# Performance work log

Measured on AMD Instinct MI355X. Metric: run time of the kernel, lower is better.

Reference implementation:

```python
import jax, jax.numpy as jnp
import numpy as np

N, E, R, B, DIN, H1, H2 = 50000, 1000000, 8, 30, 64, 64, 64


def setup_inputs() -> dict:
    key = jax.random.key(0)
    ks = jax.random.split(key, 12)
    node_features = jax.random.normal(ks[0], (N, DIN), dtype=jnp.float32)
    src = jax.random.randint(ks[1], (E,), 0, N)
    dst = jax.random.randint(ks[2], (E,), 0, N)
    edge_index = jnp.stack([src, dst]).astype(jnp.int64)
    edge_norm = jax.random.uniform(ks[3], (E,), dtype=jnp.float32)
    edge_type = jax.random.randint(ks[4], (E,), 0, R).astype(jnp.int64)
    s = 0.05  # param init scale
    basis = jax.random.normal(ks[5], (B, DIN, H1), dtype=jnp.float32) * s
    comp = jax.random.normal(ks[6], (R, B), dtype=jnp.float32) * s
    loop_weight = jax.random.normal(ks[7], (DIN, H1), dtype=jnp.float32) * s
    bias1 = jnp.zeros((H1,), dtype=jnp.float32)
    weight2 = jax.random.normal(ks[8], (H1, H2), dtype=jnp.float32) * s
    bias2 = jnp.zeros((H2,), dtype=jnp.float32)
    return dict(node_features=node_features, edge_index=edge_index,
                edge_norm=edge_norm, edge_type=edge_type, basis=basis,
                comp=comp, loop_weight=loop_weight, bias1=bias1,
                weight2=weight2, bias2=bias2)


def reference(node_features, edge_index, edge_norm, edge_type, basis, comp,
              loop_weight, bias1, weight2, bias2):
    n = node_features.shape[0]
    src, dst = edge_index[0], edge_index[1]

    # ---- RGCNConv (basis decomposition, sum aggregation, self-loop, bias) ----
    # relation weights from bases: [R, DIN, H1]
    Wrel = jnp.einsum('rb,bio->rio', comp, basis)
    # transform every node by every relation once: [N, R, H1]
    xr = jnp.einsum('ni,rio->nro', node_features, Wrel)
    # per-edge message via (src, edge_type) gather: [E, H1]
    msg = xr[src, edge_type]
    agg1 = jax.ops.segment_sum(msg, dst, num_segments=n)
    h = agg1 + node_features @ loop_weight + bias1

    # ---- GraphConv (symmetric 'both' normalization) ----
    ones = jnp.ones((src.shape[0],), dtype=h.dtype)
    deg_out = jnp.clip(jax.ops.segment_sum(ones, src, num_segments=n), 1.0, None)
    deg_in = jnp.clip(jax.ops.segment_sum(ones, dst, num_segments=n), 1.0, None)
    hs = h * jax.lax.rsqrt(deg_out)[:, None]
    agg2 = jax.ops.segment_sum(hs[src], dst, num_segments=n)
    agg2 = agg2 * jax.lax.rsqrt(deg_in)[:, None]
    out = agg2 @ weight2 + bias2
    return out
```

## Files before the change

kernel.cpp:

```cpp
#include <hip/hip_runtime.h>

#define N_NODES 50000
#define N_EDGES 1000000
#define NB      128
#define CHUNK   7813
#define NQ      8
#define QN      6256
#define NBLK2   196

#define A_PART    0
#define A_XR      0
#define A_Y2      0
#define A_DEGP    115200000
#define A_ROWPTR  115400000
#define A_BSUM    115600128
#define A_BBASE   115601024
#define A_CSR     115601920
#define A_HS      123601920
#define A_WALL    136401920

typedef unsigned int uint32;
typedef unsigned short ushort16;

__device__ inline ushort16 f2bf(float f) {
    uint32 u = __float_as_uint(f);
    return (ushort16)((u + 0x7FFFu + ((u >> 16) & 1u)) >> 16);
}
__device__ inline float bf2f(ushort16 h) {
    return __uint_as_float(((uint32)h) << 16);
}

__global__ void k_wall(const float* __restrict__ comp, const float* __restrict__ basis,
                       const float* __restrict__ loopw, float* __restrict__ Wall) {
    int idx = blockIdx.x * 256 + threadIdx.x;
    if (idx >= 9 * 4096) return;
    int r = idx >> 12, io = idx & 4095;
    float acc;
    if (r < 8) {
        acc = 0.f;
        #pragma unroll
        for (int b = 0; b < 30; ++b) acc += comp[r * 30 + b] * basis[b * 4096 + io];
    } else {
        acc = loopw[io];
    }
    Wall[idx] = acc;
}

__global__ __launch_bounds__(256) void k_hist2(const int* __restrict__ ei,
                                               uint32* __restrict__ part) {
    __shared__ __align__(16) uint32 h[QN];
    int t = threadIdx.x, b = blockIdx.x, q = blockIdx.y;
    int lo = q * QN;
    int nq = N_NODES - lo; if (nq > QN) nq = QN;
    int4* h4 = (int4*)h;
    for (int i = t; i < QN / 4; i += 256) h4[i] = make_int4(0, 0, 0, 0);
    __syncthreads();
    int e0 = b * CHUNK, e1 = e0 + CHUNK;
    if (e1 > N_EDGES) e1 = N_EDGES;
    for (int e = e0 + t; e < e1; e += 256) {
        int s = ei[e], d = ei[N_EDGES + e];
        unsigned rs = (unsigned)(s - lo), rd = (unsigned)(d - lo);
        if (rs < (unsigned)QN) atomicAdd(&h[rs], 1u);
        if (rd < (unsigned)QN) atomicAdd(&h[rd], 0x10000u);
    }
    __syncthreads();
    int4* d4 = (int4*)(part + b * N_NODES + lo);
    const int4* s4 = (const int4*)h;
    for (int i = t; i < nq / 4; i += 256) d4[i] = s4[i];
}

__global__ __launch_bounds__(256) void k_merge(const uint32* __restrict__ part,
                                               uint32* __restrict__ degp,
                                               int* __restrict__ bsum) {
    int t = threadIdx.x, v = blockIdx.x * 256 + t;
    uint32 s = 0;
    if (v < N_NODES) {
        #pragma unroll 8
        for (int b = 0; b < NB; ++b) s += part[b * N_NODES + v];
        degp[v] = s;
    }
    int din = (int)(s >> 16);
    int r = din;
    #pragma unroll
    for (int d = 1; d < 64; d <<= 1) r += __shfl_xor(r, d);
    __shared__ int wsum[4];
    int lane = t & 63, wid = t >> 6;
    if (lane == 0) wsum[wid] = r;
    __syncthreads();
    if (t == 0) bsum[blockIdx.x] = wsum[0] + wsum[1] + wsum[2] + wsum[3];
}

__global__ void k_scanb(const int* __restrict__ bsum, int* __restrict__ bbase) {
    int t = threadIdx.x;
    int v = (t < NBLK2) ? bsum[t] : 0;
    int lane = t & 63, wid = t >> 6;
    int x = v;
    #pragma unroll
    for (int d = 1; d < 64; d <<= 1) {
        int y = __shfl_up(x, d);
        if (lane >= d) x += y;
    }
    __shared__ int wsum[4];
    if (lane == 63) wsum[wid] = x;
    __syncthreads();
    int base = 0;
    for (int w = 0; w < wid; ++w) base += wsum[w];
    if (t < NBLK2) bbase[t] = base + x - v;
}

__global__ __launch_bounds__(256) void k_base(uint32* __restrict__ part,
                                              const uint32* __restrict__ degp,
                                              const int* __restrict__ bbase,
                                              int* __restrict__ rowptr) {
    int t = threadIdx.x, v = blockIdx.x * 256 + t;
    int din = (v < N_NODES) ? (int)(degp[v] >> 16) : 0;
    int lane = t & 63, wid = t >> 6;
    int x = din;
    #pragma unroll
    for (int d = 1; d < 64; d <<= 1) {
        int y = __shfl_up(x, d);
        if (lane >= d) x += y;
    }
    __shared__ int wsum[4];
    if (lane == 63) wsum[wid] = x;
    __syncthreads();
    int base = bbase[blockIdx.x];
    for (int w = 0; w < wid; ++w) base += wsum[w];
    int start = base + x - din;
    if (v < N_NODES) {
        rowptr[v] = start;
        if (v == N_NODES - 1) rowptr[N_NODES] = start + din;
        uint32 run = (uint32)start;
        for (int b = 0; b < NB; ++b) {
            uint32 p = part[b * N_NODES + v];
            part[b * N_NODES + v] = run;
            run += (p >> 16);
        }
    }
}

__global__ __launch_bounds__(256) void k_fill2(const int* __restrict__ ei,
                                               const int* __restrict__ etype,
                                               const uint32* __restrict__ fillbase,
                                               int2* __restrict__ csr) {
    __shared__ __align__(16) uint32 cur[QN];
    int t = threadIdx.x, b = blockIdx.x, q = blockIdx.y;
    int lo = q * QN;
    int nq = N_NODES - lo; if (nq > QN) nq = QN;
    const int4* s4 = (const int4*)(fillbase + b * N_NODES + lo);
    int4* c4 = (int4*)cur;
    for (int i = t; i < nq / 4; i += 256) c4[i] = s4[i];
    __syncthreads();
    int e0 = b * CHUNK, e1 = e0 + CHUNK;
    if (e1 > N_EDGES) e1 = N_EDGES;
    for (int e = e0 + t; e < e1; e += 256) {
        int d = ei[N_EDGES + e];
        unsigned rd = (unsigned)(d - lo);
        if (rd < (unsigned)QN) {
            int s = ei[e], ty = etype[e];
            uint32 pos = atomicAdd(&cur[rd], 1u);
            csr[pos] = make_int2(s * 9 + ty, s);
        }
    }
}

__global__ __launch_bounds__(256) void k_xr(const float* __restrict__ x,
                                            const float* __restrict__ Wall,
                                            ushort16* __restrict__ xr) {
    __shared__ __align__(16) float At[32 * 256];
    __shared__ __align__(16) float Wt[32 * 64];
    int t = threadIdx.x;
    int n0 = blockIdx.x * 256;
    int r = blockIdx.y;
    int og = t & 7, ng = t >> 3;
    float acc[8][8];
    #pragma unroll
    for (int i = 0; i < 8; ++i)
        #pragma unroll
        for (int j = 0; j < 8; ++j) acc[i][j] = 0.f;

    #pragma unroll
    for (int ph = 0; ph < 2; ++ph) {
        if (ph) __syncthreads();
        #pragma unroll
        for (int j = 0; j < 8; ++j) {
            int f4 = t + j * 256;
            int n = f4 >> 3, k4 = f4 & 7;
            float4 v = make_float4(0.f, 0.f, 0.f, 0.f);
            if (n0 + n < N_NODES)
                v = *(const float4*)&x[(n0 + n) * 64 + ph * 32 + k4 * 4];
            int sl = n >> 2, nl = n & 3, kb = k4 * 4;
            At[(kb + 0) * 256 + (((sl ^ ((kb + 0) & 7)) << 2) | nl)] = v.x;
            At[(kb + 1) * 256 + (((sl ^ ((kb + 1) & 7)) << 2) | nl)] = v.y;
            At[(kb + 2) * 256 + (((sl ^ ((kb + 2) & 7)) << 2) | nl)] = v.z;
            At[(kb + 3) * 256 + (((sl ^ ((kb + 3) & 7)) << 2) | nl)] = v.w;
        }
        #pragma unroll
        for (int j = 0; j < 8; ++j) {
            int f = t + j * 256;
            Wt[f] = Wall[r * 4096 + ph * 2048 + f];
        }
        __syncthreads();
        #pragma unroll 4
        for (int k = 0; k < 32; ++k) {
            int c = k & 7;
            float4 aA = *(const float4*)&At[k * 256 + (((2 * ng) ^ c) << 2)];
            float4 aB = *(const float4*)&At[k * 256 + (((2 * ng + 1) ^ c) << 2)];
            float4 w0 = *(const float4*)&Wt[k * 64 + og * 8];
            float4 w1 = *(const float4*)&Wt[k * 64 + og * 8 + 4];
            float a_[8] = {aA.x, aA.y, aA.z, aA.w, aB.x, aB.y, aB.z, aB.w};
            float w_[8] = {w0.x, w0.y, w0.z, w0.w, w1.x, w1.y, w1.z, w1.w};
            #pragma unroll
            for (int i = 0; i < 8; ++i)
                #pragma unroll
                for (int j = 0; j < 8; ++j) acc[i][j] += a_[i] * w_[j];
        }
    }
    #pragma unroll
    for (int i = 0; i < 8; ++i) {
        int n = n0 + ng * 8 + i;
        if (n < N_NODES) {
            uint4 o;
            o.x = (uint32)f2bf(acc[i][0]) | ((uint32)f2bf(acc[i][1]) << 16);
            o.y = (uint32)f2bf(acc[i][2]) | ((uint32)f2bf(acc[i][3]) << 16);
            o.z = (uint32)f2bf(acc[i][4]) | ((uint32)f2bf(acc[i][5]) << 16);
            o.w = (uint32)f2bf(acc[i][6]) | ((uint32)f2bf(acc[i][7]) << 16);
            *(uint4*)&xr[n * 576 + r * 64 + og * 8] = o;
        }
    }
}

__global__ __launch_bounds__(256) void k_agg1(const ushort16* __restrict__ xr,
                                              const int2* __restrict__ csr,
                                              const int* __restrict__ rowptr,
                                              const uint32* __restrict__ degp,
                                              const float* __restrict__ bias1,
                                              ushort16* __restrict__ hs) {
    int t = threadIdx.x;
    int wid = t >> 6, lane = t & 63;
    int v = blockIdx.x * 4 + wid;
    if (v >= N_NODES) return;
    int sub = lane >> 4, cg = lane & 15;
    float a0 = 0.f, a1 = 0.f, a2 = 0.f, a3 = 0.f;
    int end = rowptr[v + 1];
    for (int j = rowptr[v] + sub; j < end; j += 4) {
        int r0 = csr[j].x;
        uint2 u = *(const uint2*)&xr[r0 * 64 + cg * 4];
        a0 += __uint_as_float(u.x << 16);
        a1 += __uint_as_float(u.x & 0xffff0000u);
        a2 += __uint_as_float(u.y << 16);
        a3 += __uint_as_float(u.y & 0xffff0000u);
    }
    #pragma unroll
    for (int d = 16; d < 64; d <<= 1) {
        a0 += __shfl_xor(a0, d);
        a1 += __shfl_xor(a1, d);
        a2 += __shfl_xor(a2, d);
        a3 += __shfl_xor(a3, d);
    }
    uint2 slu = *(const uint2*)&xr[(v * 9 + 8) * 64 + cg * 4];
    float4 b = *(const float4*)&bias1[cg * 4];
    a0 += __uint_as_float(slu.x << 16) + b.x;
    a1 += __uint_as_float(slu.x & 0xffff0000u) + b.y;
    a2 += __uint_as_float(slu.y << 16) + b.z;
    a3 += __uint_as_float(slu.y & 0xffff0000u) + b.w;
    float dg = (float)(degp[v] & 0xffffu);
    if (dg < 1.f) dg = 1.f;
    float s = rsqrtf(dg);
    if (sub == 0) {
        uint2 o;
        o.x = (uint32)f2bf(a0 * s) | ((uint32)f2bf(a1 * s) << 16);
        o.y = (uint32)f2bf(a2 * s) | ((uint32)f2bf(a3 * s) << 16);
        *(uint2*)&hs[v * 64 + cg * 4] = o;
    }
}

__global__ __launch_bounds__(256) void k_agg2(const ushort16* __restrict__ hs,
                                              const int2* __restrict__ csr,
                                              const int* __restrict__ rowptr,
                                              const uint32* __restrict__ degp,
                                              float* __restrict__ y2) {
    int t = threadIdx.x;
    int wid = t >> 6, lane = t & 63;
    int v = blockIdx.x * 4 + wid;
    if (v >= N_NODES) return;
    int sub = lane >> 4, cg = lane & 15;
    float a0 = 0.f, a1 = 0.f, a2 = 0.f, a3 = 0.f;
    int end = rowptr[v + 1];
    for (int j = rowptr[v] + sub; j < end; j += 4) {
        int r0 = csr[j].y;
        uint2 u = *(const uint2*)&hs[r0 * 64 + cg * 4];
        a0 += __uint_as_float(u.x << 16);
        a1 += __uint_as_float(u.x & 0xffff0000u);
        a2 += __uint_as_float(u.y << 16);
        a3 += __uint_as_float(u.y & 0xffff0000u);
    }
    #pragma unroll
    for (int d = 16; d < 64; d <<= 1) {
        a0 += __shfl_xor(a0, d);
        a1 += __shfl_xor(a1, d);
        a2 += __shfl_xor(a2, d);
        a3 += __shfl_xor(a3, d);
    }
    float dg = (float)(degp[v] >> 16);
    if (dg < 1.f) dg = 1.f;
    float s = rsqrtf(dg);
    if (sub == 0) {
        *(float4*)&y2[v * 64 + cg * 4] =
            make_float4(a0 * s, a1 * s, a2 * s, a3 * s);
    }
}

__global__ __launch_bounds__(256) void k_gemm2(const float* __restrict__ y2,
                                               const float* __restrict__ w2,
                                               const float* __restrict__ bias2,
                                               float* __restrict__ out) {
    __shared__ __align__(16) float At[32 * 256];
    __shared__ __align__(16) float Wt[32 * 64];
    int t = threadIdx.x;
    int n0 = blockIdx.x * 256;
    int og = t & 7, ng = t >> 3;
    float acc[8][8];
    #pragma unroll
    for (int i = 0; i < 8; ++i)
        #pragma unroll
        for (int j = 0; j < 8; ++j) acc[i][j] = 0.f;

    #pragma unroll
    for (int ph = 0; ph < 2; ++ph) {
        if (ph) __syncthreads();
        #pragma unroll
        for (int j = 0; j < 8; ++j) {
            int f4 = t + j * 256;
            int n = f4 >> 3, k4 = f4 & 7;
            float4 v = make_float4(0.f, 0.f, 0.f, 0.f);
            if (n0 + n < N_NODES)
                v = *(const float4*)&y2[(n0 + n) * 64 + ph * 32 + k4 * 4];
            int sl = n >> 2, nl = n & 3, kb = k4 * 4;
            At[(kb + 0) * 256 + (((sl ^ ((kb + 0) & 7)) << 2) | nl)] = v.x;
            At[(kb + 1) * 256 + (((sl ^ ((kb + 1) & 7)) << 2) | nl)] = v.y;
            At[(kb + 2) * 256 + (((sl ^ ((kb + 2) & 7)) << 2) | nl)] = v.z;
            At[(kb + 3) * 256 + (((sl ^ ((kb + 3) & 7)) << 2) | nl)] = v.w;
        }
        #pragma unroll
        for (int j = 0; j < 8; ++j) {
            int f = t + j * 256;
            Wt[f] = w2[ph * 2048 + f];
        }
        __syncthreads();
        #pragma unroll 4
        for (int k = 0; k < 32; ++k) {
            int c = k & 7;
            float4 aA = *(const float4*)&At[k * 256 + (((2 * ng) ^ c) << 2)];
            float4 aB = *(const float4*)&At[k * 256 + (((2 * ng + 1) ^ c) << 2)];
            float4 w0 = *(const float4*)&Wt[k * 64 + og * 8];
            float4 w1 = *(const float4*)&Wt[k * 64 + og * 8 + 4];
            float a_[8] = {aA.x, aA.y, aA.z, aA.w, aB.x, aB.y, aB.z, aB.w};
            float w_[8] = {w0.x, w0.y, w0.z, w0.w, w1.x, w1.y, w1.z, w1.w};
            #pragma unroll
            for (int i = 0; i < 8; ++i)
                #pragma unroll
                for (int j = 0; j < 8; ++j) acc[i][j] += a_[i] * w_[j];
        }
    }
    float4 b0 = *(const float4*)&bias2[og * 8];
    float4 b1 = *(const float4*)&bias2[og * 8 + 4];
    #pragma unroll
    for (int i = 0; i < 8; ++i) {
        int n = n0 + ng * 8 + i;
        if (n < N_NODES) {
            *(float4*)&out[n * 64 + og * 8] =
                make_float4(acc[i][0] + b0.x, acc[i][1] + b0.y,
                            acc[i][2] + b0.z, acc[i][3] + b0.w);
            *(float4*)&out[n * 64 + og * 8 + 4] =
                make_float4(acc[i][4] + b1.x, acc[i][5] + b1.y,
                            acc[i][6] + b1.z, acc[i][7] + b1.w);
        }
    }
}

extern "C" void kernel_launch(void* const* d_in, const int* in_sizes, int n_in,
                              void* d_out, int out_size, void* d_ws, size_t ws_size,
                              hipStream_t stream) {
    const float* x      = (const float*)d_in[0];
    const int*   ei     = (const int*)d_in[1];
    const int*   etype  = (const int*)d_in[3];
    const float* basis  = (const float*)d_in[4];
    const float* comp   = (const float*)d_in[5];
    const float* loopw  = (const float*)d_in[6];
    const float* bias1  = (const float*)d_in[7];
    const float* w2     = (const float*)d_in[8];
    const float* bias2  = (const float*)d_in[9];
    float* out = (float*)d_out;

    char* ws = (char*)d_ws;
    uint32*   part   = (uint32*)(ws + A_PART);
    ushort16* xr     = (ushort16*)(ws + A_XR);
    float*    y2     = (float*)(ws + A_Y2);
    uint32*   degp   = (uint32*)(ws + A_DEGP);
    int*      rowptr = (int*)(ws + A_ROWPTR);
    int*      bsum   = (int*)(ws + A_BSUM);
    int*      bbase  = (int*)(ws + A_BBASE);
    int2*     csr    = (int2*)(ws + A_CSR);
    ushort16* hs     = (ushort16*)(ws + A_HS);
    float*    Wall   = (float*)(ws + A_WALL);

    k_wall<<<144, 256, 0, stream>>>(comp, basis, loopw, Wall);
    k_hist2<<<dim3(NB, NQ), 256, 0, stream>>>(ei, part);
    k_merge<<<NBLK2, 256, 0, stream>>>(part, degp, bsum);
    k_scanb<<<1, 256, 0, stream>>>(bsum, bbase);
    k_base<<<NBLK2, 256, 0, stream>>>(part, degp, bbase, rowptr);
    k_fill2<<<dim3(NB, NQ), 256, 0, stream>>>(ei, etype, part, csr);
    k_xr<<<dim3((N_NODES + 255) / 256, 9), 256, 0, stream>>>(x, Wall, xr);
    k_agg1<<<N_NODES / 4, 256, 0, stream>>>(xr, csr, rowptr, degp, bias1, hs);
    k_agg2<<<N_NODES / 4, 256, 0, stream>>>(hs, csr, rowptr, degp, y2);
    k_gemm2<<<(N_NODES + 255) / 256, 256, 0, stream>>>(y2, w2, bias2, out);
}
```

Before: 291.4 us.

## Use bf16 MFMA for per-relation node transform with pre-converted inputs

```diff
diff --git a/kernel.cpp b/kernel.cpp
--- a/kernel.cpp
+++ b/kernel.cpp
@@ -11,6 +11,7 @@
 #define A_PART    0
 #define A_XR      0
 #define A_Y2      0
+#define A_XBF     57600000
 #define A_DEGP    115200000
 #define A_ROWPTR  115400000
 #define A_BSUM    115600128
@@ -18,9 +19,10 @@
 #define A_CSR     115601920
 #define A_HS      123601920
 #define A_WALL    136401920
-
 typedef unsigned int uint32;
 typedef unsigned short ushort16;
+typedef __attribute__((ext_vector_type(8))) short bf16x8;
+typedef __attribute__((ext_vector_type(4))) float f32x4;
 
 __device__ inline ushort16 f2bf(float f) {
     uint32 u = __float_as_uint(f);
@@ -31,10 +33,11 @@
 }
 
 __global__ void k_wall(const float* __restrict__ comp, const float* __restrict__ basis,
-                       const float* __restrict__ loopw, float* __restrict__ Wall) {
+                       const float* __restrict__ loopw, ushort16* __restrict__ wallbf) {
     int idx = blockIdx.x * 256 + threadIdx.x;
     if (idx >= 9 * 4096) return;
     int r = idx >> 12, io = idx & 4095;
+    int i = io >> 6, o = io & 63;
     float acc;
     if (r < 8) {
         acc = 0.f;
@@ -43,7 +46,22 @@
     } else {
         acc = loopw[io];
     }
-    Wall[idx] = acc;
+    wallbf[r * 4096 + o * 64 + i] = f2bf(acc);
+}
+
+__global__ __launch_bounds__(256) void k_xbf(const float* __restrict__ x,
+                                             ushort16* __restrict__ xbf) {
+    int g = blockIdx.x * 256 + threadIdx.x;
+    int base = g * 8;
+    if (base >= N_NODES * 64) return;
+    float4 v0 = *(const float4*)&x[base];
+    float4 v1 = *(const float4*)&x[base + 4];
+    uint4 o;
+    o.x = (uint32)f2bf(v0.x) | ((uint32)f2bf(v0.y) << 16);
+    o.y = (uint32)f2bf(v0.z) | ((uint32)f2bf(v0.w) << 16);
+    o.z = (uint32)f2bf(v1.x) | ((uint32)f2bf(v1.y) << 16);
+    o.w = (uint32)f2bf(v1.z) | ((uint32)f2bf(v1.w) << 16);
+    *(uint4*)&xbf[base] = o;
 }
 
 __global__ __launch_bounds__(256) void k_hist2(const int* __restrict__ ei,
@@ -164,68 +182,55 @@
     }
 }
 
-__global__ __launch_bounds__(256) void k_xr(const float* __restrict__ x,
-                                            const float* __restrict__ Wall,
+__global__ __launch_bounds__(256) void k_xr(const ushort16* __restrict__ xbf,
+                                            const ushort16* __restrict__ wallbf,
                                             ushort16* __restrict__ xr) {
-    __shared__ __align__(16) float At[32 * 256];
-    __shared__ __align__(16) float Wt[32 * 64];
+    __shared__ __align__(16) ushort16 Abf[64 * 64];
+    __shared__ __align__(16) ushort16 Wbf[64 * 64];
+    __shared__ __align__(16) ushort16 Ot[64 * 64];
     int t = threadIdx.x;
-    int n0 = blockIdx.x * 256;
+    int n0 = blockIdx.x * 64;
     int r = blockIdx.y;
-    int og = t & 7, ng = t >> 3;
-    float acc[8][8];
-    #pragma unroll
-    for (int i = 0; i < 8; ++i)
+    {
+        int n = t >> 2, s0 = (t & 3) * 2;
+        uint4 v0 = make_uint4(0, 0, 0, 0), v1 = v0;
+        if (n0 + n < N_NODES) {
+            v0 = *(const uint4*)&xbf[(n0 + n) * 64 + s0 * 8];
+            v1 = *(const uint4*)&xbf[(n0 + n) * 64 + s0 * 8 + 8];
+        }
+        *(uint4*)&Abf[n * 64 + ((s0 ^ (n & 7)) * 8)]       = v0;
+        *(uint4*)&Abf[n * 64 + (((s0 + 1) ^ (n & 7)) * 8)] = v1;
+        uint4 w0 = *(const uint4*)&wallbf[r * 4096 + n * 64 + s0 * 8];
+        uint4 w1 = *(const uint4*)&wallbf[r * 4096 + n * 64 + s0 * 8 + 8];
+        *(uint4*)&Wbf[n * 64 + ((s0 ^ (n & 7)) * 8)]       = w0;
+        *(uint4*)&Wbf[n * 64 + (((s0 + 1) ^ (n & 7)) * 8)] = w1;
+    }
+    __syncthreads();
+    int w = t >> 6, l = t & 63;
+    int row = l & 15, kg = l >> 4;
+    int an = w * 16 + row;
+    bf16x8 a0 = *(const bf16x8*)&Abf[an * 64 + (((0 + kg) ^ (an & 7)) * 8)];
+    bf16x8 a1 = *(const bf16x8*)&Abf[an * 64 + (((4 + kg) ^ (an & 7)) * 8)];
+    #pragma unroll
+    for (int ct = 0; ct < 4; ++ct) {
+        int bo = ct * 16 + row;
+        bf16x8 b0 = *(const bf16x8*)&Wbf[bo * 64 + (((0 + kg) ^ (bo & 7)) * 8)];
+        bf16x8 b1 = *(const bf16x8*)&Wbf[bo * 64 + (((4 + kg) ^ (bo & 7)) * 8)];
+        f32x4 acc = {0.f, 0.f, 0.f, 0.f};
+        acc = __builtin_amdgcn_mfma_f32_16x16x32_bf16(a0, b0, acc, 0, 0, 0);
+        acc = __builtin_amdgcn_mfma_f32_16x16x32_bf16(a1, b1, acc, 0, 0, 0);
         #pragma unroll
-        for (int j = 0; j < 8; ++j) acc[i][j] = 0.f;
-
-    #pragma unroll
-    for (int ph = 0; ph < 2; ++ph) {
-        if (ph) __syncthreads();
-        #pragma unroll
-        for (int j = 0; j < 8; ++j) {
-            int f4 = t + j * 256;
-            int n = f4 >> 3, k4 = f4 & 7;
-            float4 v = make_float4(0.f, 0.f, 0.f, 0.f);
-            if (n0 + n < N_NODES)
-                v = *(const float4*)&x[(n0 + n) * 64 + ph * 32 + k4 * 4];
-            int sl = n >> 2, nl = n & 3, kb = k4 * 4;
-            At[(kb + 0) * 256 + (((sl ^ ((kb + 0) & 7)) << 2) | nl)] = v.x;
-            At[(kb + 1) * 256 + (((sl ^ ((kb + 1) & 7)) << 2) | nl)] = v.y;
-            At[(kb + 2) * 256 + (((sl ^ ((kb + 2) & 7)) << 2) | nl)] = v.z;
-            At[(kb + 3) * 256 + (((sl ^ ((kb + 3) & 7)) << 2) | nl)] = v.w;
-        }
-        #pragma unroll
-        for (int j = 0; j < 8; ++j) {
-            int f = t + j * 256;
-            Wt[f] = Wall[r * 4096 + ph * 2048 + f];
-        }
-        __syncthreads();
-        #pragma unroll 4
-        for (int k = 0; k < 32; ++k) {
-            int c = k & 7;
-            float4 aA = *(const float4*)&At[k * 256 + (((2 * ng) ^ c) << 2)];
-            float4 aB = *(const float4*)&At[k * 256 + (((2 * ng + 1) ^ c) << 2)];
-            float4 w0 = *(const float4*)&Wt[k * 64 + og * 8];
-            float4 w1 = *(const float4*)&Wt[k * 64 + og * 8 + 4];
-            float a_[8] = {aA.x, aA.y, aA.z, aA.w, aB.x, aB.y, aB.z, aB.w};
-            float w_[8] = {w0.x, w0.y, w0.z, w0.w, w1.x, w1.y, w1.z, w1.w};
-            #pragma unroll
-            for (int i = 0; i < 8; ++i)
-                #pragma unroll
-                for (int j = 0; j < 8; ++j) acc[i][j] += a_[i] * w_[j];
-        }
-    }
-    #pragma unroll
-    for (int i = 0; i < 8; ++i) {
-        int n = n0 + ng * 8 + i;
-        if (n < N_NODES) {
-            uint4 o;
-            o.x = (uint32)f2bf(acc[i][0]) | ((uint32)f2bf(acc[i][1]) << 16);
-            o.y = (uint32)f2bf(acc[i][2]) | ((uint32)f2bf(acc[i][3]) << 16);
-            o.z = (uint32)f2bf(acc[i][4]) | ((uint32)f2bf(acc[i][5]) << 16);
-            o.w = (uint32)f2bf(acc[i][6]) | ((uint32)f2bf(acc[i][7]) << 16);
-            *(uint4*)&xr[n * 576 + r * 64 + og * 8] = o;
+        for (int j = 0; j < 4; ++j)
+            Ot[(w * 16 + kg * 4 + j) * 64 + ct * 16 + row] = f2bf(acc[j]);
+    }
+    __syncthreads();
+    {
+        int n = t >> 2, s = (t & 3) * 2;
+        if (n0 + n < N_NODES) {
+            *(uint4*)&xr[(n0 + n) * 576 + r * 64 + s * 8] =
+                *(const uint4*)&Ot[n * 64 + s * 8];
+            *(uint4*)&xr[(n0 + n) * 576 + r * 64 + s * 8 + 8] =
+                *(const uint4*)&Ot[n * 64 + s * 8 + 8];
         }
     }
 }
@@ -397,21 +402,23 @@
     uint32*   part   = (uint32*)(ws + A_PART);
     ushort16* xr     = (ushort16*)(ws + A_XR);
     float*    y2     = (float*)(ws + A_Y2);
+    ushort16* xbf    = (ushort16*)(ws + A_XBF);
     uint32*   degp   = (uint32*)(ws + A_DEGP);
     int*      rowptr = (int*)(ws + A_ROWPTR);
     int*      bsum   = (int*)(ws + A_BSUM);
     int*      bbase  = (int*)(ws + A_BBASE);
     int2*     csr    = (int2*)(ws + A_CSR);
     ushort16* hs     = (ushort16*)(ws + A_HS);
-    float*    Wall   = (float*)(ws + A_WALL);
-
-    k_wall<<<144, 256, 0, stream>>>(comp, basis, loopw, Wall);
+    ushort16* wallbf = (ushort16*)(ws + A_WALL);
+
+    k_wall<<<144, 256, 0, stream>>>(comp, basis, loopw, wallbf);
+    k_xbf<<<(N_NODES * 64 / 8 + 255) / 256, 256, 0, stream>>>(x, xbf);
     k_hist2<<<dim3(NB, NQ), 256, 0, stream>>>(ei, part);
     k_merge<<<NBLK2, 256, 0, stream>>>(part, degp, bsum);
     k_scanb<<<1, 256, 0, stream>>>(bsum, bbase);
     k_base<<<NBLK2, 256, 0, stream>>>(part, degp, bbase, rowptr);
     k_fill2<<<dim3(NB, NQ), 256, 0, stream>>>(ei, etype, part, csr);
-    k_xr<<<dim3((N_NODES + 255) / 256, 9), 256, 0, stream>>>(x, Wall, xr);
+    k_xr<<<dim3((N_NODES + 63) / 64, 9), 256, 0, stream>>>(xbf, wallbf, xr);
     k_agg1<<<N_NODES / 4, 256, 0, stream>>>(xr, csr, rowptr, degp, bias1, hs);
     k_agg2<<<N_NODES / 4, 256, 0, stream>>>(hs, csr, rowptr, degp, y2);
     k_gemm2<<<(N_NODES + 255) / 256, 256, 0, stream>>>(y2, w2, bias2, out);
```

Result: faster. 260.5 us (-10.6%).
